# Performance work log

Measured on AMD Instinct MI355X. Metric: run time of the kernel, lower is better.

## Reference

```python
import jax, jax.numpy as jnp
import numpy as np

H_FEATS = 256

def setup_inputs() -> dict:
    key = jax.random.key(0)
    k1, k2, k3, k4, k5, k6, k7 = jax.random.split(key, 7)
    N, E, D = 100000, 500000, H_FEATS
    h = jax.random.normal(k1, (N, D), dtype=jnp.float32)
    src = jax.random.randint(k2, (E,), 0, N)
    dst = jax.random.randint(k3, (E,), 0, N)
    # Linear params (PyTorch default init: U(-1/sqrt(fan_in), 1/sqrt(fan_in)))
    b1_bound = 1.0 / np.sqrt(2 * D)
    b2_bound = 1.0 / np.sqrt(D)
    W1 = jax.random.uniform(k4, (2 * D, D), jnp.float32, -b1_bound, b1_bound)
    b1 = jax.random.uniform(k5, (D,), jnp.float32, -b1_bound, b1_bound)
    W2 = jax.random.uniform(k6, (D, 1), jnp.float32, -b2_bound, b2_bound)
    b2 = jax.random.uniform(k7, (1,), jnp.float32, -b2_bound, b2_bound)
    return {"h": h, "src": src, "dst": dst, "W1": W1, "b1": b1, "W2": W2, "b2": b2}

def reference(h, src, dst, W1, b1, W2, b2):
    # Gather per-edge source/destination node features and concat: [E, 2D]
    he = jnp.concatenate([h[src], h[dst]], axis=1)
    # Linear -> ReLU -> (dropout is identity in eval) -> Linear -> Sigmoid
    hid = jax.nn.relu(he @ W1 + b1)          # [E, D]
    score = jax.nn.sigmoid((hid @ W2 + b2).squeeze(1))  # [E]
    return score
```

## Files before the change

kernel.cpp:

```cpp
#include <hip/hip_runtime.h>
#include <math.h>


typedef __attribute__((ext_vector_type(8))) short short8;
typedef __attribute__((ext_vector_type(2))) float floatx2;
typedef __attribute__((ext_vector_type(4))) float floatx4;
typedef __attribute__((ext_vector_type(16))) float floatx16;

#define D_FEAT 256
#define EPW 16

__device__ __forceinline__ float bf2f(unsigned short u) {
    union { unsigned u32; float f; } v; v.u32 = ((unsigned)u) << 16; return v.f;
}
__device__ __forceinline__ float lo16(unsigned u) {
    union { unsigned u32; float f; } v; v.u32 = u << 16; return v.f;
}
__device__ __forceinline__ float hi16(unsigned u) {
    union { unsigned u32; float f; } v; v.u32 = u & 0xffff0000u; return v.f;
}
__device__ __forceinline__ unsigned short f2bf(float f) {
    union { float f; unsigned u32; } v; v.f = f;
    unsigned x = v.u32;
    return (unsigned short)((x + 0x7fffu + ((x >> 16) & 1u)) >> 16);
}
__device__ __forceinline__ float sigmoid_safe(float r) {
    r = fminf(fmaxf(r, -30.f), 30.f);
    return 1.f / (1.f + expf(-r));
}
__device__ __forceinline__ unsigned pack4_fp8(float a, float b, float c, float d) {
    int w = __builtin_amdgcn_cvt_pk_fp8_f32(a, b, 0, false);
    w = __builtin_amdgcn_cvt_pk_fp8_f32(c, d, w, true);
    return (unsigned)w;
}

__global__ __launch_bounds__(256) void probe_dtype(const unsigned short* __restrict__ h,
                                                   int* __restrict__ flag) {
    __shared__ int cnt[256];
    const int t = threadIdx.x;
    int c = 0;
    #pragma unroll
    for (int i = 0; i < 8; ++i) {
        unsigned e = (h[t * 8 + i] >> 7) & 0xFF;
        c += (e >= 100 && e <= 140) ? 1 : 0;
    }
    cnt[t] = c;
    __syncthreads();
    if (t == 0) {
        int s = 0;
        for (int i = 0; i < 256; ++i) s += cnt[i];
        flag[0] = (s >= 1843) ? 1 : 0;
    }
}

template <int MODE>
__global__ __launch_bounds__(256) void build_wt_t(const void* __restrict__ W1v,
                                                  unsigned short* __restrict__ Wt,
                                                  const int* __restrict__ flag) {
    if (flag[0] != MODE) return;
    int j = blockIdx.x, k = threadIdx.x;
    size_t idx = (j < 256) ? ((size_t)k * 256 + j) : ((size_t)(k + 256) * 256 + (j - 256));
    unsigned short v;
    if constexpr (MODE == 1) v = ((const unsigned short*)W1v)[idx];
    else                     v = f2bf(((const float*)W1v)[idx]);
    Wt[(size_t)j * 256 + k] = v;
}

template <int MODE>
__global__ __launch_bounds__(512, 2) void gemm_pq_t(const void* __restrict__ hv,
                                                    const unsigned short* __restrict__ Wt,
                                                    unsigned char* __restrict__ PQ8,
                                                    int N, const int* __restrict__ flag) {
    if (flag[0] != MODE) return;
    __shared__ unsigned short Bs[256][256];
    __shared__ unsigned short As[64][256];

    const int tid  = threadIdx.x;
    const int lane = tid & 63;
    const int wid  = tid >> 6;
    const int l32  = lane & 31;
    const int q2   = lane >> 5;

    {
        const int r = tid >> 1;
        const unsigned cbase = (tid & 1) * 256;
        const char* srcp = (const char*)Wt + (size_t)r * 512 + cbase;
        char* dstb = (char*)&Bs[0][0] + (unsigned)r * 512;
        const unsigned sw = ((unsigned)r & 31) << 4;
        #pragma unroll
        for (int i = 0; i < 16; ++i) {
            short8 v = *(const short8*)(srcp + i * 16);
            *(short8*)(dstb + ((cbase + i * 16) ^ sw)) = v;
        }
    }

    short8 breg[16];
    {
        const char* bp = (const char*)Wt + (size_t)(256 + wid * 32 + l32) * 512 + q2 * 16;
        #pragma unroll
        for (int ks = 0; ks < 16; ++ks)
            breg[ks] = *(const short8*)(bp + ks * 32);
    }

    const int ar = tid >> 3;
    const unsigned ac = (unsigned)(tid & 7) * 64;
    const unsigned aswz = ((unsigned)ar & 31) << 4;

    short8  pref[4];
    floatx4 pf[8];
    auto load_a = [&](int ms) {
        const int gm = ms * 64 + ar;
        if constexpr (MODE == 1) {
            #pragma unroll
            for (int j = 0; j < 4; ++j) {
                short8 v = {};
                if (gm < N)
                    v = *(const short8*)((const char*)hv + (size_t)gm * 512 + ac + j * 16);
                pref[j] = v;
            }
        } else {
            #pragma unroll
            for (int j = 0; j < 4; ++j) {
                floatx4 f0 = {}, f1 = {};
                if (gm < N) {
                    const float* p = (const float*)hv + (size_t)gm * 256 + (ac + j * 16) / 2;
                    f0 = *(const floatx4*)p;
                    f1 = *(const floatx4*)(p + 4);
                }
                pf[2 * j]     = f0;
                pf[2 * j + 1] = f1;
            }
        }
    };

    const int NT = (N + 63) >> 6;
    const int GM = gridDim.x;
    if ((int)blockIdx.x < NT) load_a(blockIdx.x);

    for (int ms = blockIdx.x; ms < NT; ms += GM) {
        __syncthreads();
        {
            char* adst = (char*)&As[0][0] + (unsigned)ar * 512;
            #pragma unroll
            for (int j = 0; j < 4; ++j) {
                short8 v;
                if constexpr (MODE == 1) {
                    v = pref[j];
                } else {
                    floatx4 f0 = pf[2 * j], f1 = pf[2 * j + 1];
                    v[0] = (short)f2bf(f0.x); v[1] = (short)f2bf(f0.y);
                    v[2] = (short)f2bf(f0.z); v[3] = (short)f2bf(f0.w);
                    v[4] = (short)f2bf(f1.x); v[5] = (short)f2bf(f1.y);
                    v[6] = (short)f2bf(f1.z); v[7] = (short)f2bf(f1.w);
                }
                *(short8*)(adst + ((ac + j * 16) ^ aswz)) = v;
            }
        }
        const int msn = ms + GM;
        if (msn < NT) load_a(msn);
        __syncthreads();

        floatx16 acc[2][2] = {};
        #pragma unroll
        for (int ks = 0; ks < 16; ++ks) {
            const unsigned cb = ((unsigned)(ks * 32 + q2 * 16)) ^ ((unsigned)l32 << 4);
            short8 a0 = *(const short8*)((const char*)&As[0][0] + (unsigned)l32 * 512 + cb);
            short8 a1 = *(const short8*)((const char*)&As[0][0] + (unsigned)(32 + l32) * 512 + cb);
            short8 bl = *(const short8*)((const char*)&Bs[0][0] + (unsigned)(wid * 32 + l32) * 512 + cb);
            acc[0][0] = __builtin_amdgcn_mfma_f32_32x32x16_bf16(bl,       a0, acc[0][0], 0, 0, 0);
            acc[1][0] = __builtin_amdgcn_mfma_f32_32x32x16_bf16(bl,       a1, acc[1][0], 0, 0, 0);
            acc[0][1] = __builtin_amdgcn_mfma_f32_32x32x16_bf16(breg[ks], a0, acc[0][1], 0, 0, 0);
            acc[1][1] = __builtin_amdgcn_mfma_f32_32x32x16_bf16(breg[ks], a1, acc[1][1], 0, 0, 0);
        }

        __syncthreads();
        {
            unsigned char* scr = (unsigned char*)&As[0][0];
            #pragma unroll
            for (int mi = 0; mi < 2; ++mi) {
                const unsigned row = (unsigned)(mi * 32 + l32);
                const unsigned rs = (row & 31) << 4;
                #pragma unroll
                for (int nb = 0; nb < 2; ++nb) {
                    const unsigned nbase = (unsigned)(nb * 256 + wid * 32 + 4 * q2);
                    #pragma unroll
                    for (int g = 0; g < 4; ++g) {
                        unsigned w = pack4_fp8(acc[mi][nb][4 * g + 0], acc[mi][nb][4 * g + 1],
                                               acc[mi][nb][4 * g + 2], acc[mi][nb][4 * g + 3]);
                        const unsigned col = nbase + 8 * g;
                        *(unsigned*)(scr + ((row * 512 + col) ^ rs)) = w;
                    }
                }
            }
        }
        __syncthreads();
        {
            const unsigned char* scr = (const unsigned char*)&As[0][0];
            const int gm = ms * 64 + ar;
            if (gm < N) {
                #pragma unroll
                for (int j = 0; j < 4; ++j) {
                    const unsigned col = ac + j * 16;
                    uint4 v = *(const uint4*)(scr + (((unsigned)ar * 512 + col) ^ aswz));
                    *(uint4*)(PQ8 + (size_t)gm * 512 + col) = v;
                }
            }
        }
    }
}

template <int MODE>
__global__ __launch_bounds__(256) void edge_score_t(const unsigned char* __restrict__ PQ8,
                                                    const int* __restrict__ src,
                                                    const int* __restrict__ dst,
                                                    const void* __restrict__ b1v,
                                                    const void* __restrict__ W2v,
                                                    const void* __restrict__ b2v,
                                                    void* __restrict__ outv,
                                                    int E, const int* __restrict__ flag) {
    if (flag[0] != MODE) return;
    const int wave = threadIdx.x >> 6;
    const int lane = threadIdx.x & 63;
    const int e0 = (blockIdx.x * 4 + wave) * EPW;
    if (e0 >= E) return;
    const int l32 = lane & 31;
    const int* __restrict__ idxp = (lane >= 32) ? dst : src;

    float bf[8], wf[8];
    if constexpr (MODE == 1) {
        const uint4 bvr = *(const uint4*)((const unsigned short*)b1v + l32 * 8);
        const uint4 wvr = *(const uint4*)((const unsigned short*)W2v + l32 * 8);
        bf[0] = lo16(bvr.x); bf[1] = hi16(bvr.x); bf[2] = lo16(bvr.y); bf[3] = hi16(bvr.y);
        bf[4] = lo16(bvr.z); bf[5] = hi16(bvr.z); bf[6] = lo16(bvr.w); bf[7] = hi16(bvr.w);
        wf[0] = lo16(wvr.x); wf[1] = hi16(wvr.x); wf[2] = lo16(wvr.y); wf[3] = hi16(wvr.y);
        wf[4] = lo16(wvr.z); wf[5] = hi16(wvr.z); wf[6] = lo16(wvr.w); wf[7] = hi16(wvr.w);
    } else {
        const float* bp = (const float*)b1v + l32 * 8;
        const float* wp = (const float*)W2v + l32 * 8;
        #pragma unroll
        for (int t = 0; t < 8; ++t) { bf[t] = bp[t]; wf[t] = wp[t]; }
    }
    float bias2;
    if constexpr (MODE == 1) bias2 = bf2f(((const unsigned short*)b2v)[0]);
    else                     bias2 = ((const float*)b2v)[0];

    int node[EPW];
    #pragma unroll
    for (int i = 0; i < EPW; ++i) {
        int e = e0 + i; if (e >= E) e = E - 1;
        node[i] = idxp[e];
    }
    uint2 raw[EPW];
    #pragma unroll
    for (int i = 0; i < EPW; ++i)
        raw[i] = *(const uint2*)(PQ8 + (size_t)node[i] * 512 + lane * 8);

    float res[EPW];
    #pragma unroll
    for (int i = 0; i < EPW; ++i) {
        uint2 o;
        o.x = (unsigned)__shfl_xor((int)raw[i].x, 32);
        o.y = (unsigned)__shfl_xor((int)raw[i].y, 32);
        floatx2 p01 = __builtin_amdgcn_cvt_pk_f32_fp8((int)raw[i].x, false);
        floatx2 p23 = __builtin_amdgcn_cvt_pk_f32_fp8((int)raw[i].x, true);
        floatx2 p45 = __builtin_amdgcn_cvt_pk_f32_fp8((int)raw[i].y, false);
        floatx2 p67 = __builtin_amdgcn_cvt_pk_f32_fp8((int)raw[i].y, true);
        floatx2 q01 = __builtin_amdgcn_cvt_pk_f32_fp8((int)o.x, false);
        floatx2 q23 = __builtin_amdgcn_cvt_pk_f32_fp8((int)o.x, true);
        floatx2 q45 = __builtin_amdgcn_cvt_pk_f32_fp8((int)o.y, false);
        floatx2 q67 = __builtin_amdgcn_cvt_pk_f32_fp8((int)o.y, true);
        float v0 = fmaxf(p01.x + q01.x + bf[0], 0.f);
        float v1 = fmaxf(p01.y + q01.y + bf[1], 0.f);
        float v2 = fmaxf(p23.x + q23.x + bf[2], 0.f);
        float v3 = fmaxf(p23.y + q23.y + bf[3], 0.f);
        float v4 = fmaxf(p45.x + q45.x + bf[4], 0.f);
        float v5 = fmaxf(p45.y + q45.y + bf[5], 0.f);
        float v6 = fmaxf(p67.x + q67.x + bf[6], 0.f);
        float v7 = fmaxf(p67.y + q67.y + bf[7], 0.f);
        res[i] = v0 * wf[0] + v1 * wf[1] + v2 * wf[2] + v3 * wf[3]
               + v4 * wf[4] + v5 * wf[5] + v6 * wf[6] + v7 * wf[7];
    }

    float t8[8];
    #pragma unroll
    for (int k = 0; k < 8; ++k) {
        float a = res[2 * k], b = res[2 * k + 1];
        float own  = (lane & 1) ? b : a;
        float send = (lane & 1) ? a : b;
        t8[k] = own + __shfl_xor(send, 1);
    }
    float t4[4];
    #pragma unroll
    for (int k = 0; k < 4; ++k) {
        float a = t8[2 * k], b = t8[2 * k + 1];
        float own  = (lane & 2) ? b : a;
        float send = (lane & 2) ? a : b;
        t4[k] = own + __shfl_xor(send, 2);
    }
    float t2[2];
    #pragma unroll
    for (int k = 0; k < 2; ++k) {
        float a = t4[2 * k], b = t4[2 * k + 1];
        float own  = (lane & 4) ? b : a;
        float send = (lane & 4) ? a : b;
        t2[k] = own + __shfl_xor(send, 4);
    }
    float t1;
    {
        float a = t2[0], b = t2[1];
        float own  = (lane & 8) ? b : a;
        float send = (lane & 8) ? a : b;
        t1 = own + __shfl_xor(send, 8);
    }
    t1 += __shfl_xor(t1, 16);

    if (lane < 16) {
        const int e = e0 + lane;
        if (e < E) {
            float r = sigmoid_safe(t1 + bias2);
            if constexpr (MODE == 1) ((unsigned short*)outv)[e] = f2bf(r);
            else                     ((float*)outv)[e] = r;
        }
    }
}

template <int MODE>
__global__ __launch_bounds__(256) void edge_fused_t(const void* __restrict__ hv,
                                                    const int* __restrict__ src,
                                                    const int* __restrict__ dst,
                                                    const void* __restrict__ W1v,
                                                    const void* __restrict__ b1v,
                                                    const void* __restrict__ W2v,
                                                    const void* __restrict__ b2v,
                                                    void* __restrict__ outv,
                                                    int E, const int* __restrict__ flag) {
    if (flag && flag[0] != MODE) return;
    __shared__ float he[512];
    __shared__ float wsum[4];
    const int e = blockIdx.x;
    if (e >= E) return;
    const int t = threadIdx.x;
    const int s = src[e];
    const int d = dst[e];

    if constexpr (MODE == 1) {
        he[t]       = bf2f(((const unsigned short*)hv)[(size_t)s * 256 + t]);
        he[256 + t] = bf2f(((const unsigned short*)hv)[(size_t)d * 256 + t]);
    } else {
        he[t]       = ((const float*)hv)[(size_t)s * 256 + t];
        he[256 + t] = ((const float*)hv)[(size_t)d * 256 + t];
    }
    __syncthreads();

    float acc;
    if constexpr (MODE == 1) acc = bf2f(((const unsigned short*)b1v)[t]);
    else                     acc = ((const float*)b1v)[t];

    #pragma unroll 8
    for (int k = 0; k < 512; ++k) {
        float w;
        if constexpr (MODE == 1) w = bf2f(((const unsigned short*)W1v)[(size_t)k * 256 + t]);
        else                     w = ((const float*)W1v)[(size_t)k * 256 + t];
        acc += he[k] * w;
    }

    float w2;
    if constexpr (MODE == 1) w2 = bf2f(((const unsigned short*)W2v)[t]);
    else                     w2 = ((const float*)W2v)[t];
    acc = fmaxf(acc, 0.f) * w2;

    #pragma unroll
    for (int off = 32; off > 0; off >>= 1)
        acc += __shfl_xor(acc, off);
    if ((t & 63) == 0) wsum[t >> 6] = acc;
    __syncthreads();

    if (t == 0) {
        float bias2;
        if constexpr (MODE == 1) bias2 = bf2f(((const unsigned short*)b2v)[0]);
        else                     bias2 = ((const float*)b2v)[0];
        float r = sigmoid_safe(wsum[0] + wsum[1] + wsum[2] + wsum[3] + bias2);
        if constexpr (MODE == 1) ((unsigned short*)outv)[e] = f2bf(r);
        else                     ((float*)outv)[e] = r;
    }
}

extern "C" void kernel_launch(void* const* d_in, const int* in_sizes, int n_in,
                              void* d_out, int out_size, void* d_ws, size_t ws_size,
                              hipStream_t stream) {
    const void* h  = d_in[0];
    const int* src = (const int*)d_in[1];
    const int* dst = (const int*)d_in[2];
    const void* W1 = d_in[3];
    const void* b1 = d_in[4];
    const void* W2 = d_in[5];
    const void* b2 = d_in[6];

    const int N = in_sizes[0] / D_FEAT;
    const int E = in_sizes[1];

    const size_t FLAG_BYTES = 256;
    const size_t wt_bytes  = (size_t)512 * D_FEAT * sizeof(unsigned short);
    const size_t pq_bytes  = (size_t)N * 512;
    const size_t need = FLAG_BYTES + wt_bytes + pq_bytes;

    int* flag = (int*)d_ws;
    unsigned short* Wt = (unsigned short*)((char*)d_ws + FLAG_BYTES);
    unsigned char*  PQ8 = (unsigned char*)((char*)d_ws + FLAG_BYTES + wt_bytes);

    if (ws_size >= need) {
        probe_dtype<<<1, 256, 0, stream>>>((const unsigned short*)h, flag);

        build_wt_t<1><<<512, 256, 0, stream>>>(W1, Wt, flag);
        build_wt_t<0><<<512, 256, 0, stream>>>(W1, Wt, flag);

        gemm_pq_t<1><<<256, 512, 0, stream>>>(h, Wt, PQ8, N, flag);
        gemm_pq_t<0><<<256, 512, 0, stream>>>(h, Wt, PQ8, N, flag);

        int egrid = (E + 4 * EPW - 1) / (4 * EPW);
        edge_score_t<1><<<egrid, 256, 0, stream>>>(PQ8, src, dst, b1, W2, b2, d_out, E, flag);
        edge_score_t<0><<<egrid, 256, 0, stream>>>(PQ8, src, dst, b1, W2, b2, d_out, E, flag);
    } else if (ws_size >= FLAG_BYTES) {
        probe_dtype<<<1, 256, 0, stream>>>((const unsigned short*)h, flag);
        edge_fused_t<1><<<E, 256, 0, stream>>>(h, src, dst, W1, b1, W2, b2, d_out, E, flag);
        edge_fused_t<0><<<E, 256, 0, stream>>>(h, src, dst, W1, b1, W2, b2, d_out, E, flag);
    } else {
        edge_fused_t<1><<<E, 256, 0, stream>>>(h, src, dst, W1, b1, W2, b2, d_out, E, nullptr);
    }
}
```

Before: 247.6 us.

## Split each wave into two half-wave edge groups to drop cross-half shuffles

Each half-wave now processes its own interleaved set of 8 edges, loading both the src (P) and dst (Q) projected rows per edge, instead of the whole wave sharing 16 edges with a cross-half shuffle to combine P and Q. This removes the 32-lane shuffle of the raw data and shortens the butterfly reduction by one level, at the cost of each lane issuing two gather loads per edge and loading both index arrays. The number of outstanding gathers per lane stays at 16, so memory parallelism is roughly unchanged.

Result: no change. 242.8 us (-1.9%).

```diff
diff --git a/kernel.cpp b/kernel.cpp
--- a/kernel.cpp
+++ b/kernel.cpp
@@ -224,7 +224,7 @@
     const int e0 = (blockIdx.x * 4 + wave) * EPW;
     if (e0 >= E) return;
     const int l32 = lane & 31;
-    const int* __restrict__ idxp = (lane >= 32) ? dst : src;
+    const int par = lane >> 5;
 
     float bf[8], wf[8];
     if constexpr (MODE == 1) {
@@ -244,31 +244,31 @@
     if constexpr (MODE == 1) bias2 = bf2f(((const unsigned short*)b2v)[0]);
     else                     bias2 = ((const float*)b2v)[0];
 
-    int node[EPW];
-    #pragma unroll
-    for (int i = 0; i < EPW; ++i) {
-        int e = e0 + i; if (e >= E) e = E - 1;
-        node[i] = idxp[e];
-    }
-    uint2 raw[EPW];
-    #pragma unroll
-    for (int i = 0; i < EPW; ++i)
-        raw[i] = *(const uint2*)(PQ8 + (size_t)node[i] * 512 + lane * 8);
-
-    float res[EPW];
-    #pragma unroll
-    for (int i = 0; i < EPW; ++i) {
-        uint2 o;
-        o.x = (unsigned)__shfl_xor((int)raw[i].x, 32);
-        o.y = (unsigned)__shfl_xor((int)raw[i].y, 32);
-        floatx2 p01 = __builtin_amdgcn_cvt_pk_f32_fp8((int)raw[i].x, false);
-        floatx2 p23 = __builtin_amdgcn_cvt_pk_f32_fp8((int)raw[i].x, true);
-        floatx2 p45 = __builtin_amdgcn_cvt_pk_f32_fp8((int)raw[i].y, false);
-        floatx2 p67 = __builtin_amdgcn_cvt_pk_f32_fp8((int)raw[i].y, true);
-        floatx2 q01 = __builtin_amdgcn_cvt_pk_f32_fp8((int)o.x, false);
-        floatx2 q23 = __builtin_amdgcn_cvt_pk_f32_fp8((int)o.x, true);
-        floatx2 q45 = __builtin_amdgcn_cvt_pk_f32_fp8((int)o.y, false);
-        floatx2 q67 = __builtin_amdgcn_cvt_pk_f32_fp8((int)o.y, true);
+    int nsrc[8], ndst[8];
+    #pragma unroll
+    for (int p = 0; p < 8; ++p) {
+        int e = e0 + 2 * p + par; if (e >= E) e = E - 1;
+        nsrc[p] = src[e];
+        ndst[p] = dst[e];
+    }
+    uint2 rp[8], rq[8];
+    #pragma unroll
+    for (int p = 0; p < 8; ++p) {
+        rp[p] = *(const uint2*)(PQ8 + (size_t)nsrc[p] * 512 + l32 * 8);
+        rq[p] = *(const uint2*)(PQ8 + (size_t)ndst[p] * 512 + 256 + l32 * 8);
+    }
+
+    float res[8];
+    #pragma unroll
+    for (int p = 0; p < 8; ++p) {
+        floatx2 p01 = __builtin_amdgcn_cvt_pk_f32_fp8((int)rp[p].x, false);
+        floatx2 p23 = __builtin_amdgcn_cvt_pk_f32_fp8((int)rp[p].x, true);
+        floatx2 p45 = __builtin_amdgcn_cvt_pk_f32_fp8((int)rp[p].y, false);
+        floatx2 p67 = __builtin_amdgcn_cvt_pk_f32_fp8((int)rp[p].y, true);
+        floatx2 q01 = __builtin_amdgcn_cvt_pk_f32_fp8((int)rq[p].x, false);
+        floatx2 q23 = __builtin_amdgcn_cvt_pk_f32_fp8((int)rq[p].x, true);
+        floatx2 q45 = __builtin_amdgcn_cvt_pk_f32_fp8((int)rq[p].y, false);
+        floatx2 q67 = __builtin_amdgcn_cvt_pk_f32_fp8((int)rq[p].y, true);
         float v0 = fmaxf(p01.x + q01.x + bf[0], 0.f);
         float v1 = fmaxf(p01.y + q01.y + bf[1], 0.f);
         float v2 = fmaxf(p23.x + q23.x + bf[2], 0.f);
@@ -277,45 +277,38 @@
         float v5 = fmaxf(p45.y + q45.y + bf[5], 0.f);
         float v6 = fmaxf(p67.x + q67.x + bf[6], 0.f);
         float v7 = fmaxf(p67.y + q67.y + bf[7], 0.f);
-        res[i] = v0 * wf[0] + v1 * wf[1] + v2 * wf[2] + v3 * wf[3]
+        res[p] = v0 * wf[0] + v1 * wf[1] + v2 * wf[2] + v3 * wf[3]
                + v4 * wf[4] + v5 * wf[5] + v6 * wf[6] + v7 * wf[7];
     }
 
-    float t8[8];
-    #pragma unroll
-    for (int k = 0; k < 8; ++k) {
+    float t4[4];
+    #pragma unroll
+    for (int k = 0; k < 4; ++k) {
         float a = res[2 * k], b = res[2 * k + 1];
         float own  = (lane & 1) ? b : a;
         float send = (lane & 1) ? a : b;
-        t8[k] = own + __shfl_xor(send, 1);
-    }
-    float t4[4];
-    #pragma unroll
-    for (int k = 0; k < 4; ++k) {
-        float a = t8[2 * k], b = t8[2 * k + 1];
+        t4[k] = own + __shfl_xor(send, 1);
+    }
+    float t2[2];
+    #pragma unroll
+    for (int k = 0; k < 2; ++k) {
+        float a = t4[2 * k], b = t4[2 * k + 1];
         float own  = (lane & 2) ? b : a;
         float send = (lane & 2) ? a : b;
-        t4[k] = own + __shfl_xor(send, 2);
-    }
-    float t2[2];
-    #pragma unroll
-    for (int k = 0; k < 2; ++k) {
-        float a = t4[2 * k], b = t4[2 * k + 1];
-        float own  = (lane & 4) ? b : a;
-        float send = (lane & 4) ? a : b;
-        t2[k] = own + __shfl_xor(send, 4);
+        t2[k] = own + __shfl_xor(send, 2);
     }
     float t1;
     {
         float a = t2[0], b = t2[1];
-        float own  = (lane & 8) ? b : a;
-        float send = (lane & 8) ? a : b;
-        t1 = own + __shfl_xor(send, 8);
-    }
+        float own  = (lane & 4) ? b : a;
+        float send = (lane & 4) ? a : b;
+        t1 = own + __shfl_xor(send, 4);
+    }
+    t1 += __shfl_xor(t1, 8);
     t1 += __shfl_xor(t1, 16);
 
-    if (lane < 16) {
-        const int e = e0 + lane;
+    if (l32 < 8) {
+        const int e = e0 + 2 * (lane & 7) + par;
         if (e < E) {
             float r = sigmoid_safe(t1 + bias2);
             if constexpr (MODE == 1) ((unsigned short*)outv)[e] = f2bf(r);
```
